# Performance work log

Hardware: AMD Instinct MI355X
Metric: run time of the kernel (lower is better)

The kernel has to match this reference:

```python
import jax, jax.numpy as jnp
import numpy as np

B, DIM, H, W = 8, 128, 64, 64
C, DI, N, R, K = DIM // 4, 2 * (DIM // 4), 16, 2, 4  # chunk dim, d_inner, d_state, dt_rank, n_dirs
L = H * W
EPS = 1e-5


def dwconv(x, w, b, dil):
    # x: [B,C,H,W]; w: [C,1,kh,kw] depthwise; torch padding='same' with dilation
    y = jax.lax.conv_general_dilated(
        x, w, window_strides=(1, 1), padding='SAME', rhs_dilation=(dil, dil),
        dimension_numbers=('NCHW', 'OIHW', 'NCHW'), feature_group_count=x.shape[1])
    return y + b[None, :, None, None]


def layernorm(x, w, b):
    mu = jnp.mean(x, -1, keepdims=True)
    var = jnp.var(x, -1, keepdims=True)
    return (x - mu) * jax.lax.rsqrt(var + EPS) * w + b


def axial_dw(x, mh_w, mh_b, mw_w, mw_b, c_w, c_b, dil):
    skip = x
    x = dwconv(x, mw_w, mw_b, dil)   # (1,7) kernel
    x = dwconv(x, mh_w, mh_b, dil)   # (7,1) kernel
    x = dwconv(x, c_w, c_b, dil)     # 3x3 kernel
    return x + skip


def ss2d(x, in_proj_w, conv_w, conv_b, x_proj_w, dt_proj_w, dt_proj_b,
         A_log, D, out_norm_w, out_norm_b, out_proj_w):
    # x: [B,H,W,C] channels-last (VMamba SS2D)
    b, h, w, _ = x.shape
    xz = jnp.einsum('bhwc,ec->bhwe', x, in_proj_w)          # [B,H,W,2*DI]
    xc, z = jnp.split(xz, 2, axis=-1)
    xc = xc.transpose(0, 3, 1, 2)                           # [B,DI,H,W]
    xc = jax.nn.silu(dwconv(xc, conv_w, conv_b, 1))
    l = h * w
    x_hw = xc.reshape(b, DI, l)
    x_wh = xc.transpose(0, 1, 3, 2).reshape(b, DI, l)
    xs = jnp.stack([x_hw, x_wh], 1)                         # [B,2,DI,L]
    xs = jnp.concatenate([xs, jnp.flip(xs, -1)], 1)         # [B,4,DI,L]
    x_dbl = jnp.einsum('bkdl,kcd->bkcl', xs, x_proj_w)      # c = R+2N
    dts, Bs, Cs = x_dbl[:, :, :R], x_dbl[:, :, R:R + N], x_dbl[:, :, R + N:]
    dts = jnp.einsum('bkrl,kdr->bkdl', dts, dt_proj_w)
    delta = jax.nn.softplus(dts + dt_proj_b[None, :, :, None])  # [B,4,DI,L]
    A = -jnp.exp(A_log)                                     # [4,DI,N]

    def step(hst, inp):
        u_t, dt_t, B_t, C_t = inp  # [B,4,DI],[B,4,DI],[B,4,N],[B,4,N]
        dA = jnp.exp(dt_t[..., None] * A)                   # [B,4,DI,N]
        hst = hst * dA + (dt_t * u_t)[..., None] * B_t[:, :, None, :]
        y = jnp.einsum('bkdn,bkn->bkd', hst, C_t)
        return hst, y

    u_l = jnp.moveaxis(xs, -1, 0)
    dt_l = jnp.moveaxis(delta, -1, 0)
    B_l = jnp.moveaxis(Bs, -1, 0)
    C_l = jnp.moveaxis(Cs, -1, 0)
    h0 = jnp.zeros((b, K, DI, N), xc.dtype)
    _, ys = jax.lax.scan(step, h0, (u_l, dt_l, B_l, C_l))   # [L,B,4,DI]
    out_y = jnp.moveaxis(ys, 0, -1) + D[None, :, :, None] * xs  # [B,4,DI,L]

    inv_y = jnp.flip(out_y[:, 2:4], -1)
    wh_y = out_y[:, 1].reshape(b, DI, w, h).transpose(0, 1, 3, 2).reshape(b, DI, l)
    invwh_y = inv_y[:, 1].reshape(b, DI, w, h).transpose(0, 1, 3, 2).reshape(b, DI, l)
    y = out_y[:, 0] + inv_y[:, 0] + wh_y + invwh_y          # [B,DI,L]
    y = y.transpose(0, 2, 1).reshape(b, h, w, DI)
    y = layernorm(y, out_norm_w, out_norm_b)
    y = y * jax.nn.silu(z)
    return jnp.einsum('bhwd,cd->bhwc', y, out_proj_w)


def setup_inputs() -> dict:
    key = jax.random.key(0)
    ks = iter(jax.random.split(key, 64))
    nrm = lambda s, sc=0.05: jax.random.normal(next(ks), s, jnp.float32) * sc
    inp = {'x': jax.random.normal(next(ks), (B, DIM, H, W), jnp.float32)}
    for i in (1, 2, 3):
        inp[f'dw{i}_mh_w'] = nrm((C, 1, 7, 1), 0.1); inp[f'dw{i}_mh_b'] = nrm((C,), 0.02)
        inp[f'dw{i}_mw_w'] = nrm((C, 1, 1, 7), 0.1); inp[f'dw{i}_mw_b'] = nrm((C,), 0.02)
        inp[f'dw{i}_c_w'] = nrm((C, 1, 3, 3), 0.1); inp[f'dw{i}_c_b'] = nrm((C,), 0.02)
    inp['ln_w'] = jnp.ones((C,)); inp['ln_b'] = jnp.zeros((C,))
    inp['in_proj_w'] = nrm((2 * DI, C))
    inp['conv_w'] = nrm((DI, 1, 3, 3), 0.1); inp['conv_b'] = nrm((DI,), 0.02)
    inp['x_proj_w'] = nrm((K, R + 2 * N, DI))
    inp['dt_proj_w'] = nrm((K, DI, R), 0.1)
    inp['dt_proj_b'] = nrm((K, DI), 0.02)
    inp['A_log'] = jax.random.uniform(next(ks), (K, DI, N), jnp.float32, 0.0, 2.0)
    inp['D'] = jnp.ones((K, DI), jnp.float32)
    inp['out_norm_w'] = jnp.ones((DI,)); inp['out_norm_b'] = jnp.zeros((DI,))
    inp['out_proj_w'] = nrm((C, DI))
    inp['bn_g'] = jnp.ones((DIM,)); inp['bn_b'] = jnp.zeros((DIM,))
    inp['bn_m'] = jnp.zeros((DIM,)); inp['bn_v'] = jnp.ones((DIM,))
    return inp


def reference(x, dw1_mh_w, dw1_mh_b, dw1_mw_w, dw1_mw_b, dw1_c_w, dw1_c_b,
              dw2_mh_w, dw2_mh_b, dw2_mw_w, dw2_mw_b, dw2_c_w, dw2_c_b,
              dw3_mh_w, dw3_mh_b, dw3_mw_w, dw3_mw_b, dw3_c_w, dw3_c_b,
              ln_w, ln_b, in_proj_w, conv_w, conv_b, x_proj_w, dt_proj_w, dt_proj_b,
              A_log, D, out_norm_w, out_norm_b, out_proj_w, bn_g, bn_b, bn_m, bn_v):
    def vss(xc):  # shared VSSBlock: [B,C,H,W] -> [B,C,H,W]
        t = xc.transpose(0, 2, 3, 1)
        t = t + ss2d(layernorm(t, ln_w, ln_b), in_proj_w, conv_w, conv_b, x_proj_w,
                     dt_proj_w, dt_proj_b, A_log, D, out_norm_w, out_norm_b, out_proj_w)
        return t.transpose(0, 3, 1, 2)

    x1, x2, x3, x4 = jnp.split(x, 4, axis=1)
    x1 = vss(axial_dw(x1, dw1_mh_w, dw1_mh_b, dw1_mw_w, dw1_mw_b, dw1_c_w, dw1_c_b, 1))
    x2 = vss(axial_dw(x2, dw2_mh_w, dw2_mh_b, dw2_mw_w, dw2_mw_b, dw2_c_w, dw2_c_b, 2))
    x3 = vss(axial_dw(x3, dw3_mh_w, dw3_mh_b, dw3_mw_w, dw3_mw_b, dw3_c_w, dw3_c_b, 3))
    xc = jnp.concatenate([x1, x2, x3, x4], axis=1)
    # BatchNorm2d in inference mode (running stats)
    y = (xc - bn_m[None, :, None, None]) * jax.lax.rsqrt(bn_v + EPS)[None, :, None, None]
    y = y * bn_g[None, :, None, None] + bn_b[None, :, None, None]
    return jax.nn.relu(y)
```

## Files before the change

### kernel.cpp

```cpp
#include <hip/hip_runtime.h>
#include <math.h>

#define LB __launch_bounds__(256)
#define LB512 __launch_bounds__(512)

#define LOG2E 1.44269504088896340736f
static __device__ __forceinline__ float silu_f(float x){ return x / (1.f + __expf(-x)); }
static __device__ __forceinline__ float softplus_f(float x){
    return (x > 20.f) ? x : __logf(1.f + __expf(x));
}

struct AxialArgs { const float* w[18]; };

__global__ LB void axial_kernel(const float* __restrict__ x, AxialArgs args,
    float* __restrict__ acc,
    const float* __restrict__ bn_g, const float* __restrict__ bn_b,
    const float* __restrict__ bn_m, const float* __restrict__ bn_v,
    float* __restrict__ out)
{
    __shared__ float s0[4096];
    __shared__ float s1[4096];
    if (blockIdx.x >= 768){
        const int gid = (blockIdx.x - 768)*256 + threadIdx.x;
        const int e = gid*4;
        const int l = e & 4095, bc = e >> 12;
        const int c = bc & 31, b = bc >> 5;
        const int ch = 96 + c;
        const size_t idx = ((size_t)b*128+ch)*4096 + l;
        float4 v = *(const float4*)&x[idx];
        const float sc = rsqrtf(bn_v[ch]+1e-5f)*bn_g[ch];
        const float mb = bn_m[ch], bbv = bn_b[ch];
        v.x = fmaxf((v.x-mb)*sc+bbv, 0.f);
        v.y = fmaxf((v.y-mb)*sc+bbv, 0.f);
        v.z = fmaxf((v.z-mb)*sc+bbv, 0.f);
        v.w = fmaxf((v.w-mb)*sc+bbv, 0.f);
        *(float4*)&out[idx] = v;
        return;
    }
    const int chunk = blockIdx.x >> 8;
    const int bc = blockIdx.x & 255;
    const int b = bc >> 5, c = bc & 31;
    const int dil = chunk + 1;
    const float* mh_w = args.w[chunk*6+0];
    const float* mh_b = args.w[chunk*6+1];
    const float* mw_w = args.w[chunk*6+2];
    const float* mw_b = args.w[chunk*6+3];
    const float* cw   = args.w[chunk*6+4];
    const float* cb   = args.w[chunk*6+5];
    const int tid = threadIdx.x;
    const float* xin = x + ((size_t)(b*128 + chunk*32 + c)) * 4096;
    float orig[16];
    #pragma unroll
    for (int kk=0;kk<16;++kk){ float v=xin[tid+kk*256]; orig[kk]=v; s0[tid+kk*256]=v; }
    __syncthreads();

    float w7[7];
    #pragma unroll
    for (int t=0;t<7;++t) w7[t]=mw_w[c*7+t];
    float bias = mw_b[c];
    float v[16];
    #pragma unroll
    for (int kk=0;kk<16;++kk){
        int p=tid+kk*256, i=p>>6, j=p&63;
        float s=bias;
        #pragma unroll
        for (int t=0;t<7;++t){ int jj=j+(t-3)*dil; if (jj>=0&&jj<64) s+=s0[i*64+jj]*w7[t]; }
        v[kk]=s;
    }
    #pragma unroll
    for (int kk=0;kk<16;++kk) s1[tid+kk*256]=v[kk];
    __syncthreads();

    #pragma unroll
    for (int t=0;t<7;++t) w7[t]=mh_w[c*7+t];
    bias = mh_b[c];
    #pragma unroll
    for (int kk=0;kk<16;++kk){
        int p=tid+kk*256, i=p>>6, j=p&63;
        float s=bias;
        #pragma unroll
        for (int t=0;t<7;++t){ int ii=i+(t-3)*dil; if (ii>=0&&ii<64) s+=s1[ii*64+j]*w7[t]; }
        v[kk]=s;
    }
    __syncthreads();
    #pragma unroll
    for (int kk=0;kk<16;++kk) s0[tid+kk*256]=v[kk];
    __syncthreads();

    float w9[9];
    #pragma unroll
    for (int t=0;t<9;++t) w9[t]=cw[c*9+t];
    bias = cb[c];
    float* aout = acc + (size_t)chunk*1048576 + ((size_t)(b*32+c))*4096;
    #pragma unroll
    for (int kk=0;kk<16;++kk){
        int p=tid+kk*256, i=p>>6, j=p&63;
        float s=bias;
        #pragma unroll
        for (int a=0;a<3;++a){
            int ii=i+(a-1)*dil; if (ii<0||ii>=64) continue;
            #pragma unroll
            for (int bb2=0;bb2<3;++bb2){
                int jj=j+(bb2-1)*dil; if (jj<0||jj>=64) continue;
                s += s0[ii*64+jj]*w9[a*3+bb2];
            }
        }
        aout[p] = s + orig[kk];
    }
}

__global__ LB512 void lnproj_kernel(const float* __restrict__ acc, int ch0, size_t cs,
    const float* __restrict__ ln_w, const float* __restrict__ ln_b,
    const float* __restrict__ in_proj_w,
    float* __restrict__ xc, float* __restrict__ z)
{
    __shared__ float s_a[32*65];
    const int cl = blockIdx.x >> 9;
    const int local = blockIdx.x & 511;
    const int chunk = ch0 + cl;
    const int b = local >> 6, lt = local & 63;
    const int l0 = lt*64;
    const int tid = threadIdx.x;
    const float* ab = acc + (size_t)chunk*1048576 + (size_t)b*32*4096 + l0;
    for (int i=tid;i<2048;i+=512){ int c=i>>6, j=i&63; s_a[c*65+j]=ab[(size_t)c*4096 + j]; }
    __syncthreads();
    const int l = tid & 63;
    const int g = __builtin_amdgcn_readfirstlane(tid >> 6);
    float v[32];
    float mu=0.f;
    #pragma unroll
    for (int c=0;c<32;++c){ v[c]=s_a[c*65+l]; mu+=v[c]; }
    mu *= (1.f/32.f);
    float var=0.f;
    #pragma unroll
    for (int c=0;c<32;++c){ float d2=v[c]-mu; var+=d2*d2; }
    var *= (1.f/32.f);
    float rs = rsqrtf(var+1e-5f);
    #pragma unroll
    for (int c=0;c<32;++c) v[c] = (v[c]-mu)*rs*ln_w[c] + ln_b[c];
    float* xcp = xc + (size_t)cl*cs + (size_t)b*64*4096 + l0 + l;
    float* zp  = z  + (size_t)cl*cs + (size_t)b*64*4096 + l0 + l;
    for (int e=g*16; e<g*16+16; ++e){
        const float* wr = in_proj_w + e*32;
        float s=0.f;
        #pragma unroll
        for (int c=0;c<32;++c) s += wr[c]*v[c];
        if (e<64) xcp[(size_t)e*4096]=s; else zp[(size_t)(e-64)*4096]=s;
    }
}

__global__ LB void conv3_kernel(const float* __restrict__ xc, size_t cs,
    const float* __restrict__ conv_w, const float* __restrict__ conv_b,
    float* __restrict__ xconv, float* __restrict__ xconvT)
{
    __shared__ float s0[4096];
    __shared__ float s1[64*65];
    const int cl = blockIdx.x >> 9;
    const int bd = blockIdx.x & 511;
    const int d = bd & 63;
    const int tid = threadIdx.x;
    const float* in = xc + (size_t)cl*cs + (size_t)bd*4096;
    #pragma unroll
    for (int kk=0;kk<16;++kk) s0[tid+kk*256]=in[tid+kk*256];
    __syncthreads();
    float w9[9];
    #pragma unroll
    for (int t=0;t<9;++t) w9[t]=conv_w[d*9+t];
    float bias = conv_b[d];
    float* outp = xconv + (size_t)cl*cs + (size_t)bd*4096;
    #pragma unroll
    for (int kk=0;kk<16;++kk){
        int p=tid+kk*256, i=p>>6, j=p&63;
        float s=bias;
        #pragma unroll
        for (int a=0;a<3;++a){
            int ii=i+a-1; if (ii<0||ii>=64) continue;
            #pragma unroll
            for (int bb2=0;bb2<3;++bb2){
                int jj=j+bb2-1; if (jj<0||jj>=64) continue;
                s += s0[ii*64+jj]*w9[a*3+bb2];
            }
        }
        s = silu_f(s);
        outp[p]=s;
        s1[i*65+j]=s;
    }
    __syncthreads();
    float* outT = xconvT + (size_t)cl*cs + (size_t)bd*4096;
    #pragma unroll
    for (int kk=0;kk<16;++kk){ int p=tid+kk*256; outT[p] = s1[(p&63)*65 + (p>>6)]; }
}

__global__ LB void projscan1_kernel(const float* __restrict__ xconv, const float* __restrict__ xconvT,
    size_t cs,
    const float* __restrict__ x_proj_w, const float* __restrict__ dt_proj_w,
    const float* __restrict__ dt_proj_b, const float* __restrict__ A_log,
    float* __restrict__ Bsb, float* __restrict__ Csb, float* __restrict__ dts_g,
    float* __restrict__ Ssum, float* __restrict__ hloc)
{
    __shared__ float s_x[64*65];
    __shared__ float s_dlt[64*65];
    __shared__ __align__(16) float s_B[1024];
    __shared__ float s_dts[128];
    __shared__ float s_Spart[4][64];
    float* s_C = s_dlt;
    const int cl = blockIdx.x >> 11;
    const int blkL = blockIdx.x & 2047;
    const int g = blkL & 63, bk = blkL >> 6;
    const int k = bk & 3, b = bk >> 2;
    const int tid = threadIdx.x;
    const int t0 = g*64;
    const float* src = ((k & 1) ? xconvT : xconv) + (size_t)cl*cs;
    const float* sb = src + (size_t)b*64*4096;
    for (int i=tid;i<4096;i+=256){
        int d=i>>6, j=i&63;
        int col = (k&2) ? (4095-(t0+j)) : (t0+j);
        s_x[j*65+d] = sb[(size_t)d*4096 + col];
    }
    __syncthreads();

    {
        const int t = tid & 63;
        const int q = __builtin_amdgcn_readfirstlane(tid >> 6);
        const float* wp = x_proj_w + k*2176;
        float acc9[9];
        #pragma unroll
        for (int r=0;r<9;++r) acc9[r]=0.f;
        const int r0 = q*9;
        const int nr = (q==3)?7:9;
        for (int ch=0; ch<4; ++ch){
            float xv[16];
            #pragma unroll
            for (int i=0;i<16;++i) xv[i] = s_x[t*65 + ch*16 + i];
            #pragma unroll
            for (int r=0;r<9;++r){
                if (r < nr){
                    const float* wr = wp + (r0+r)*64 + ch*16;
                    float s=0.f;
                    #pragma unroll
                    for (int i=0;i<16;++i) s += wr[i]*xv[i];
                    acc9[r] += s;
                }
            }
        }
        #pragma unroll
        for (int r=0;r<9;++r){
            if (r<nr){
                int row = r0 + r;
                if (row < 2)       s_dts[t*2 + row]      = acc9[r];
                else if (row < 18) s_B[t*16 + (row-2)]   = acc9[r];
                else               s_C[t*16 + (row-18)]  = acc9[r];
            }
        }
    }
    __syncthreads();

    {
        float* BsbC = Bsb + (size_t)cl*cs;
        float* CsbC = Csb + (size_t)cl*cs;
        const size_t tb = (size_t)blkL*1024;
        for (int i=tid;i<1024;i+=256){ BsbC[tb+i]=s_B[i]; CsbC[tb+i]=s_C[i]; }
        if (tid<128) (dts_g + (size_t)cl*cs)[(size_t)blkL*128 + tid] = s_dts[tid];
    }
    __syncthreads();

    {
        const int d_ = tid & 63, part = tid >> 6;
        const float w0 = dt_proj_w[k*128 + d_*2], w1 = dt_proj_w[k*128 + d_*2 + 1];
        const float bb = dt_proj_b[k*64 + d_];
        float Sp = 0.f;
        #pragma unroll
        for (int i=0;i<16;++i){
            const int t = part*16 + i;
            float dlt = softplus_f(s_dts[t*2]*w0 + s_dts[t*2+1]*w1 + bb);
            s_dlt[t*65 + d_] = dlt;
            s_x[t*65 + d_] *= dlt;
            Sp += dlt;
        }
        s_Spart[part][d_] = Sp;
    }
    __syncthreads();
    if (tid < 64){
        (Ssum + (size_t)cl*cs)[(size_t)blkL*64 + tid] =
            s_Spart[0][tid]+s_Spart[1][tid]+s_Spart[2][tid]+s_Spart[3][tid];
    }

    const int d = tid & 63;
    const int w = __builtin_amdgcn_readfirstlane(tid >> 6);
    float4 Av = *(const float4*)(A_log + ((size_t)(k*64+d)*16 + w*4));
    const float A0 = -__expf(Av.x)*LOG2E, A1 = -__expf(Av.y)*LOG2E,
                A2 = -__expf(Av.z)*LOG2E, A3 = -__expf(Av.w)*LOG2E;
    float h0=0,h1=0,h2=0,h3=0;
    #pragma unroll 4
    for (int t=0;t<64;++t){
        float dlt = s_dlt[t*65+d];
        float du  = s_x[t*65+d];
        float4 Bv = *(const float4*)&s_B[t*16 + w*4];
        h0 = h0*exp2f(dlt*A0) + du*Bv.x;
        h1 = h1*exp2f(dlt*A1) + du*Bv.y;
        h2 = h2*exp2f(dlt*A2) + du*Bv.z;
        h3 = h3*exp2f(dlt*A3) + du*Bv.w;
    }
    ((float4*)(hloc + (size_t)cl*cs))[(size_t)blkL*256 + d*4 + w] = make_float4(h0,h1,h2,h3);
}

__global__ LB void scan2_kernel(const float* __restrict__ Ssum, size_t cs,
    const float* __restrict__ hloc, const float* __restrict__ A_log,
    float* __restrict__ hin)
{
    const int cl = blockIdx.x >> 7;
    const int j = (blockIdx.x & 127)*256 + threadIdx.x;
    const int bk = j >> 10, dn = j & 1023;
    const int k = bk & 3, d = dn >> 4, n = dn & 15;
    const float* SsC = Ssum + (size_t)cl*cs;
    const float* hlC = hloc + (size_t)cl*cs;
    float* hinC = hin + (size_t)cl*cs;
    const float A = -__expf(A_log[(size_t)(k*64+d)*16 + n]) * LOG2E;
    float h = 0.f;
    #pragma unroll 4
    for (int g=0; g<64; ++g){
        const size_t o = ((size_t)bk*64 + g)*1024 + dn;
        hinC[o] = h;
        float S = SsC[((size_t)bk*64 + g)*64 + d];
        h = exp2f(A*S)*h + hlC[o];
    }
}

__global__ LB void scan3_kernel(const float* __restrict__ xconv, const float* __restrict__ xconvT,
    size_t cs,
    const float* __restrict__ Bsb, const float* __restrict__ Csb,
    const float* __restrict__ dts_g,
    const float* __restrict__ dt_proj_w, const float* __restrict__ dt_proj_b,
    const float* __restrict__ A_log, const float* __restrict__ Dp,
    const float* __restrict__ hin, float* __restrict__ outy)
{
    __shared__ __align__(16) float s_B[4][1024];
    __shared__ __align__(16) float s_C[4][1024];
    __shared__ __align__(8) float s_dts[4][128];
    __shared__ float s_y[4][64*17];
    const int cl = blockIdx.x >> 9;
    const int w = threadIdx.x >> 6;
    const int lane = threadIdx.x & 63;
    const int tile = (blockIdx.x & 511)*4 + w;
    const int g = tile & 63, bk = tile >> 6;
    const int k = bk & 3, b = bk >> 2;

    {
        const float4* B4 = (const float4*)(Bsb + (size_t)cl*cs + (size_t)tile*1024);
        const float4* C4 = (const float4*)(Csb + (size_t)cl*cs + (size_t)tile*1024);
        float4* sB4 = (float4*)s_B[w];
        float4* sC4 = (float4*)s_C[w];
        #pragma unroll
        for (int qq=0;qq<4;++qq){ sB4[lane+64*qq]=B4[lane+64*qq]; sC4[lane+64*qq]=C4[lane+64*qq]; }
        const float* dtsC = dts_g + (size_t)cl*cs;
        s_dts[w][lane]      = dtsC[(size_t)tile*128 + lane];
        s_dts[w][lane+64]   = dtsC[(size_t)tile*128 + lane + 64];
    }
    const int d = lane;
    float A[16];
    {
        const float4* Ab = (const float4*)(A_log + (size_t)(k*64+d)*16);
        #pragma unroll
        for (int qq=0;qq<4;++qq){
            float4 v = Ab[qq];
            A[qq*4+0]=-__expf(v.x)*LOG2E; A[qq*4+1]=-__expf(v.y)*LOG2E;
            A[qq*4+2]=-__expf(v.z)*LOG2E; A[qq*4+3]=-__expf(v.w)*LOG2E;
        }
    }
    float h[16];
    {
        const float4* hb = (const float4*)(hin + (size_t)cl*cs + (size_t)tile*1024 + d*16);
        #pragma unroll
        for (int qq=0;qq<4;++qq){
            float4 v=hb[qq];
            h[qq*4+0]=v.x; h[qq*4+1]=v.y; h[qq*4+2]=v.z; h[qq*4+3]=v.w;
        }
    }
    const float w0 = dt_proj_w[k*128 + d*2], w1 = dt_proj_w[k*128 + d*2 + 1];
    const float bb = dt_proj_b[k*64 + d];
    const float Dv = Dp[k*64 + d];
    const float* up = ((k&1)?xconvT:xconv) + (size_t)cl*cs + (size_t)(b*64+d)*4096;
    const float4* sB4 = (const float4*)s_B[w];
    const float4* sC4 = (const float4*)s_C[w];
    float* syw = s_y[w];
    float* obase = outy + (size_t)cl*cs + (size_t)(bk*64)*4096 + g*64;

    for (int t4=0; t4<16; ++t4){
        float u4[4];
        if (k & 2){
            float4 r = *(const float4*)(up + (4092 - g*64 - t4*4));
            u4[0]=r.w; u4[1]=r.z; u4[2]=r.y; u4[3]=r.x;
        } else {
            float4 r = *(const float4*)(up + g*64 + t4*4);
            u4[0]=r.x; u4[1]=r.y; u4[2]=r.z; u4[3]=r.w;
        }
        #pragma unroll
        for (int j=0;j<4;++j){
            const int t = t4*4 + j;
            float2 dtv = *(const float2*)&s_dts[w][t*2];
            float dlt = softplus_f(dtv.x*w0 + dtv.y*w1 + bb);
            float du  = dlt * u4[j];
            float y = 0.f;
            #pragma unroll
            for (int qq=0;qq<4;++qq){
                float4 Bv = sB4[t*4+qq];
                float4 Cv = sC4[t*4+qq];
                h[qq*4+0] = h[qq*4+0]*exp2f(dlt*A[qq*4+0]) + du*Bv.x;
                h[qq*4+1] = h[qq*4+1]*exp2f(dlt*A[qq*4+1]) + du*Bv.y;
                h[qq*4+2] = h[qq*4+2]*exp2f(dlt*A[qq*4+2]) + du*Bv.z;
                h[qq*4+3] = h[qq*4+3]*exp2f(dlt*A[qq*4+3]) + du*Bv.w;
                y += h[qq*4+0]*Cv.x + h[qq*4+1]*Cv.y + h[qq*4+2]*Cv.z + h[qq*4+3]*Cv.w;
            }
            syw[d*17 + (t & 15)] = y + Dv*u4[j];
        }
        if ((t4 & 3) == 3){
            const int tb = t4 >> 2;
            #pragma unroll
            for (int qq=0;qq<16;++qq){
                int i = qq*64 + lane;
                int dd = i >> 4, jj = i & 15;
                obase[(size_t)dd*4096 + tb*16 + jj] = syw[dd*17 + jj];
            }
        }
    }
}

__global__ LB void reduce4_kernel(const float* __restrict__ outy, size_t cs,
                                  float* __restrict__ ysum)
{
    __shared__ float s1[64*65];
    __shared__ float s3[64*65];
    const int cl = blockIdx.x >> 9;
    const int local = blockIdx.x & 511;
    const int b = local >> 6, d = local & 63;
    const int tid = threadIdx.x;
    const float* oy = outy + (size_t)cl*cs;
    const float* o0 = oy + ((size_t)((b*4+0)*64 + d))*4096;
    const float* o1 = oy + ((size_t)((b*4+1)*64 + d))*4096;
    const float* o2 = oy + ((size_t)((b*4+2)*64 + d))*4096;
    const float* o3 = oy + ((size_t)((b*4+3)*64 + d))*4096;
    #pragma unroll
    for (int it=0; it<16; ++it){
        int p = tid + it*256;
        s1[(p>>6)*65 + (p&63)] = o1[p];
        s3[(p>>6)*65 + (p&63)] = o3[p];
    }
    __syncthreads();
    float* ys = ysum + (size_t)cl*cs + ((size_t)(b*64 + d))*4096;
    #pragma unroll
    for (int it=0; it<16; ++it){
        int p = tid + it*256;
        int i = p >> 6, j = p & 63;
        ys[p] = o0[p] + o2[4095-p] + s1[j*65 + i] + s3[(63-j)*65 + (63-i)];
    }
}

__global__ LB512 void combine_kernel(const float* __restrict__ ysum, int ch0, size_t cs,
    const float* __restrict__ z, const float* __restrict__ acc,
    const float* __restrict__ onw, const float* __restrict__ onb,
    const float* __restrict__ opw,
    const float* __restrict__ bn_g, const float* __restrict__ bn_b,
    const float* __restrict__ bn_m, const float* __restrict__ bn_v,
    float* __restrict__ out)
{
    __shared__ float s_red[2][8][64];
    __shared__ float s_y[64*65];
    const int cl = blockIdx.x >> 9;
    const int chunk = ch0 + cl;
    const int local = blockIdx.x & 511;
    const int b = local >> 6, lt = local & 63;
    const int l0 = lt*64;
    const int tid = threadIdx.x;
    const int l = tid & 63;
    const int g = __builtin_amdgcn_readfirstlane(tid >> 6);
    const float* ys = ysum + (size_t)cl*cs + (size_t)b*64*4096;
    const int lf = l0 + l;
    float y[8];
    float psum=0.f, psq=0.f;
    #pragma unroll
    for (int i=0;i<8;++i){
        int d = g*8+i;
        float vv = ys[(size_t)d*4096 + lf];
        y[i]=vv; psum+=vv; psq+=vv*vv;
    }
    s_red[0][g][l]=psum; s_red[1][g][l]=psq;
    __syncthreads();
    float mu=0.f, vsum=0.f;
    #pragma unroll
    for (int gg=0;gg<8;++gg){ mu += s_red[0][gg][l]; vsum += s_red[1][gg][l]; }
    mu *= (1.f/64.f);
    float var = vsum*(1.f/64.f) - mu*mu;
    float rs = rsqrtf(var + 1e-5f);
    const float* zp = z + (size_t)cl*cs + (size_t)b*64*4096 + lf;
    #pragma unroll
    for (int i=0;i<8;++i){
        int d = g*8+i;
        float t2 = (y[i]-mu)*rs*onw[d] + onb[d];
        float zv = zp[(size_t)d*4096];
        s_y[l*65 + d] = t2 * silu_f(zv);
    }
    __syncthreads();
    float a4[4] = {0.f,0.f,0.f,0.f};
    for (int d=0; d<64; ++d){
        float xval = s_y[l*65+d];
        #pragma unroll
        for (int j=0;j<4;++j) a4[j] += opw[(g*4+j)*64+d]*xval;
    }
    const float* ap = acc + (size_t)chunk*1048576 + (size_t)b*32*4096 + lf;
    #pragma unroll
    for (int j=0;j<4;++j){
        int c = g*4+j, ch = chunk*32 + c;
        float s = a4[j] + ap[(size_t)c*4096];
        float bnv = (s - bn_m[ch])*rsqrtf(bn_v[ch]+1e-5f)*bn_g[ch] + bn_b[ch];
        out[((size_t)b*128+ch)*4096 + lf] = fmaxf(bnv, 0.f);
    }
}

extern "C" void kernel_launch(void* const* d_in, const int* in_sizes, int n_in,
                              void* d_out, int out_size, void* d_ws, size_t ws_size,
                              hipStream_t stream) {
    const float* x         = (const float*)d_in[0];
    const float* ln_w      = (const float*)d_in[19];
    const float* ln_b      = (const float*)d_in[20];
    const float* in_proj_w = (const float*)d_in[21];
    const float* conv_w    = (const float*)d_in[22];
    const float* conv_b    = (const float*)d_in[23];
    const float* x_proj_w  = (const float*)d_in[24];
    const float* dt_proj_w = (const float*)d_in[25];
    const float* dt_proj_b = (const float*)d_in[26];
    const float* A_log     = (const float*)d_in[27];
    const float* Dp        = (const float*)d_in[28];
    const float* onw       = (const float*)d_in[29];
    const float* onb       = (const float*)d_in[30];
    const float* opw       = (const float*)d_in[31];
    const float* bn_g      = (const float*)d_in[32];
    const float* bn_b      = (const float*)d_in[33];
    const float* bn_m      = (const float*)d_in[34];
    const float* bn_v      = (const float*)d_in[35];
    float* out = (float*)d_out;

    const size_t F_OUTY = 0;
    const size_t F_XC   = 0;
    const size_t F_HLO  = 2097152;
    const size_t F_Z    = 8388608;
    const size_t F_XCV  = 10485760;
    const size_t F_XCVT = 12582912;
    const size_t F_BSB  = 14680064;
    const size_t F_CSB  = 16777216;
    const size_t F_DTS  = 18874368;
    const size_t F_SSUM = 19136512;
    const size_t F_HIN  = 19267584;
    const size_t CSF    = 21364736;

    float* ws = (float*)d_ws;
    float* acc  = ws;
    float* pool = acc + 3145728;

    const size_t ws_f = ws_size / sizeof(float);
    int nch_max = 1;
    if (ws_f >= 3145728 + 3*CSF) nch_max = 3;
    else if (ws_f >= 3145728 + 2*CSF) nch_max = 2;

    float* xc     = pool + F_XC;
    float* z      = pool + F_Z;
    float* xconv  = pool + F_XCV;
    float* xconvT = pool + F_XCVT;
    float* Bsb    = pool + F_BSB;
    float* Csb    = pool + F_CSB;
    float* dts_g  = pool + F_DTS;
    float* Ssum   = pool + F_SSUM;
    float* hlo    = pool + F_HLO;
    float* hin    = pool + F_HIN;
    float* outy   = pool + F_OUTY;
    float* ysum   = pool + F_XCV;

    AxialArgs aargs;
    for (int chunk=0; chunk<3; ++chunk)
        for (int jj=0; jj<6; ++jj)
            aargs.w[chunk*6+jj] = (const float*)d_in[1 + chunk*6 + jj];
    axial_kernel<<<768+1024, 256, 0, stream>>>(x, aargs, acc, bn_g, bn_b, bn_m, bn_v, out);

    int done = 0;
    while (done < 3){
        const int nch = (3 - done < nch_max) ? (3 - done) : nch_max;
        const size_t cs = (nch > 1) ? CSF : 0;
        const int ch0 = done;

        lnproj_kernel<<<nch*512, 512, 0, stream>>>(acc, ch0, cs, ln_w, ln_b, in_proj_w, xc, z);
        conv3_kernel<<<nch*512, 256, 0, stream>>>(xc, cs, conv_w, conv_b, xconv, xconvT);
        projscan1_kernel<<<nch*2048, 256, 0, stream>>>(xconv, xconvT, cs,
                                                       x_proj_w, dt_proj_w, dt_proj_b,
                                                       A_log, Bsb, Csb, dts_g, Ssum, hlo);
        scan2_kernel<<<nch*128, 256, 0, stream>>>(Ssum, cs, hlo, A_log, hin);
        scan3_kernel<<<nch*512, 256, 0, stream>>>(xconv, xconvT, cs, Bsb, Csb, dts_g,
                                                  dt_proj_w, dt_proj_b, A_log, Dp, hin, outy);
        reduce4_kernel<<<nch*512, 256, 0, stream>>>(outy, cs, ysum);
        combine_kernel<<<nch*512, 512, 0, stream>>>(ysum, ch0, cs, z, acc, onw, onb, opw,
                                                    bn_g, bn_b, bn_m, bn_v, out);
        done += nch;
    }
}
```

Before: 456.5 us.

## Merge flipped-direction scan outputs via atomics, shrink outy and scan2 blocks

scan3 now accumulates each flipped direction's output straight into the unflipped layout with atomicAdd, so only two direction buffers need to be stored. This halves the outy buffer and lets reduce4 read two planes instead of four, with outy zeroed by a memset before each scan3. It also pads the B/C staging in projscan1 to a stride of 17 to avoid LDS bank conflicts, and splits scan2 into 64-thread blocks for more parallelism. The trade-off is atomic contention plus an extra memset pass.

New measurement: 431.7 us. -5.4%, faster.

```diff
diff --git a/kernel.cpp b/kernel.cpp
--- a/kernel.cpp
+++ b/kernel.cpp
@@ -3,6 +3,7 @@
 
 #define LB __launch_bounds__(256)
 #define LB512 __launch_bounds__(512)
+#define LB64 __launch_bounds__(64)
 
 #define LOG2E 1.44269504088896340736f
 static __device__ __forceinline__ float silu_f(float x){ return x / (1.f + __expf(-x)); }
@@ -203,7 +204,8 @@
     __shared__ __align__(16) float s_B[1024];
     __shared__ float s_dts[128];
     __shared__ float s_Spart[4][64];
-    float* s_C = s_dlt;
+    float* s_Bp = s_dlt;
+    float* s_Cp = s_dlt + 1152;
     const int cl = blockIdx.x >> 11;
     const int blkL = blockIdx.x & 2047;
     const int g = blkL & 63, bk = blkL >> 6;
@@ -247,9 +249,9 @@
         for (int r=0;r<9;++r){
             if (r<nr){
                 int row = r0 + r;
-                if (row < 2)       s_dts[t*2 + row]      = acc9[r];
-                else if (row < 18) s_B[t*16 + (row-2)]   = acc9[r];
-                else               s_C[t*16 + (row-18)]  = acc9[r];
+                if (row < 2)       s_dts[t*2 + row]       = acc9[r];
+                else if (row < 18) s_Bp[t*17 + (row-2)]   = acc9[r];
+                else               s_Cp[t*17 + (row-18)]  = acc9[r];
             }
         }
     }
@@ -259,7 +261,12 @@
         float* BsbC = Bsb + (size_t)cl*cs;
         float* CsbC = Csb + (size_t)cl*cs;
         const size_t tb = (size_t)blkL*1024;
-        for (int i=tid;i<1024;i+=256){ BsbC[tb+i]=s_B[i]; CsbC[tb+i]=s_C[i]; }
+        for (int i=tid;i<1024;i+=256){
+            int a = (i>>4)*17 + (i&15);
+            float bv = s_Bp[a], cv = s_Cp[a];
+            BsbC[tb+i]=bv; CsbC[tb+i]=cv;
+            s_B[i]=bv;
+        }
         if (tid<128) (dts_g + (size_t)cl*cs)[(size_t)blkL*128 + tid] = s_dts[tid];
     }
     __syncthreads();
@@ -304,12 +311,12 @@
     ((float4*)(hloc + (size_t)cl*cs))[(size_t)blkL*256 + d*4 + w] = make_float4(h0,h1,h2,h3);
 }
 
-__global__ LB void scan2_kernel(const float* __restrict__ Ssum, size_t cs,
+__global__ LB64 void scan2_kernel(const float* __restrict__ Ssum, size_t cs,
     const float* __restrict__ hloc, const float* __restrict__ A_log,
     float* __restrict__ hin)
 {
-    const int cl = blockIdx.x >> 7;
-    const int j = (blockIdx.x & 127)*256 + threadIdx.x;
+    const int cl = blockIdx.x >> 9;
+    const int j = (blockIdx.x & 511)*64 + threadIdx.x;
     const int bk = j >> 10, dn = j & 1023;
     const int k = bk & 3, d = dn >> 4, n = dn & 15;
     const float* SsC = Ssum + (size_t)cl*cs;
@@ -383,7 +390,7 @@
     const float4* sB4 = (const float4*)s_B[w];
     const float4* sC4 = (const float4*)s_C[w];
     float* syw = s_y[w];
-    float* obase = outy + (size_t)cl*cs + (size_t)(bk*64)*4096 + g*64;
+    float* obase = outy + (size_t)cl*cs + (size_t)((b*2 + (k&1))*64)*4096;
 
     for (int t4=0; t4<16; ++t4){
         float u4[4];
@@ -415,11 +422,22 @@
         }
         if ((t4 & 3) == 3){
             const int tb = t4 >> 2;
-            #pragma unroll
-            for (int qq=0;qq<16;++qq){
-                int i = qq*64 + lane;
-                int dd = i >> 4, jj = i & 15;
-                obase[(size_t)dd*4096 + tb*16 + jj] = syw[dd*17 + jj];
+            if (k & 2){
+                const int colr0 = 4095 - g*64 - tb*16;
+                #pragma unroll
+                for (int qq=0;qq<16;++qq){
+                    int i = qq*64 + lane;
+                    int dd = i >> 4, jj = i & 15;
+                    atomicAdd(&obase[(size_t)dd*4096 + colr0 - jj], syw[dd*17 + jj]);
+                }
+            } else {
+                const int col0 = g*64 + tb*16;
+                #pragma unroll
+                for (int qq=0;qq<16;++qq){
+                    int i = qq*64 + lane;
+                    int dd = i >> 4, jj = i & 15;
+                    atomicAdd(&obase[(size_t)dd*4096 + col0 + jj], syw[dd*17 + jj]);
+                }
             }
         }
     }
@@ -429,21 +447,17 @@
                                   float* __restrict__ ysum)
 {
     __shared__ float s1[64*65];
-    __shared__ float s3[64*65];
     const int cl = blockIdx.x >> 9;
     const int local = blockIdx.x & 511;
     const int b = local >> 6, d = local & 63;
     const int tid = threadIdx.x;
     const float* oy = outy + (size_t)cl*cs;
-    const float* o0 = oy + ((size_t)((b*4+0)*64 + d))*4096;
-    const float* o1 = oy + ((size_t)((b*4+1)*64 + d))*4096;
-    const float* o2 = oy + ((size_t)((b*4+2)*64 + d))*4096;
-    const float* o3 = oy + ((size_t)((b*4+3)*64 + d))*4096;
+    const float* m0 = oy + ((size_t)((b*2+0)*64 + d))*4096;
+    const float* m1 = oy + ((size_t)((b*2+1)*64 + d))*4096;
     #pragma unroll
     for (int it=0; it<16; ++it){
         int p = tid + it*256;
-        s1[(p>>6)*65 + (p&63)] = o1[p];
-        s3[(p>>6)*65 + (p&63)] = o3[p];
+        s1[(p>>6)*65 + (p&63)] = m1[p];
     }
     __syncthreads();
     float* ys = ysum + (size_t)cl*cs + ((size_t)(b*64 + d))*4096;
@@ -451,7 +465,7 @@
     for (int it=0; it<16; ++it){
         int p = tid + it*256;
         int i = p >> 6, j = p & 63;
-        ys[p] = o0[p] + o2[4095-p] + s1[j*65 + i] + s3[(63-j)*65 + (63-i)];
+        ys[p] = m0[p] + s1[j*65 + i];
     }
 }
 
@@ -542,15 +556,15 @@
     const size_t F_OUTY = 0;
     const size_t F_XC   = 0;
     const size_t F_HLO  = 2097152;
-    const size_t F_Z    = 8388608;
-    const size_t F_XCV  = 10485760;
-    const size_t F_XCVT = 12582912;
-    const size_t F_BSB  = 14680064;
-    const size_t F_CSB  = 16777216;
-    const size_t F_DTS  = 18874368;
-    const size_t F_SSUM = 19136512;
-    const size_t F_HIN  = 19267584;
-    const size_t CSF    = 21364736;
+    const size_t F_Z    = 4194304;
+    const size_t F_XCV  = 6291456;
+    const size_t F_XCVT = 8388608;
+    const size_t F_BSB  = 10485760;
+    const size_t F_CSB  = 12582912;
+    const size_t F_DTS  = 14680064;
+    const size_t F_SSUM = 14942208;
+    const size_t F_HIN  = 15073280;
+    const size_t CSF    = 17170432;
 
     float* ws = (float*)d_ws;
     float* acc  = ws;
@@ -591,7 +605,9 @@
         projscan1_kernel<<<nch*2048, 256, 0, stream>>>(xconv, xconvT, cs,
                                                        x_proj_w, dt_proj_w, dt_proj_b,
                                                        A_log, Bsb, Csb, dts_g, Ssum, hlo);
-        scan2_kernel<<<nch*128, 256, 0, stream>>>(Ssum, cs, hlo, A_log, hin);
+        scan2_kernel<<<nch*512, 64, 0, stream>>>(Ssum, cs, hlo, A_log, hin);
+        for (int cl2=0; cl2<nch; ++cl2)
+            hipMemsetAsync(outy + (size_t)cl2*cs, 0, (size_t)4194304*sizeof(float), stream);
         scan3_kernel<<<nch*512, 256, 0, stream>>>(xconv, xconvT, cs, Bsb, Csb, dts_g,
                                                   dt_proj_w, dt_proj_b, A_log, Dp, hin, outy);
         reduce4_kernel<<<nch*512, 256, 0, stream>>>(outy, cs, ysum);
```
